# Performance work log

Hardware: AMD Instinct MI355X
Metric: run time of the kernel (lower is better)

Reference implementation:

```python
import jax, jax.numpy as jnp
import numpy as np

LN_EPS = 1e-5

def _layernorm(x, g, b):
    mu = jnp.mean(x, axis=-1, keepdims=True)
    var = jnp.var(x, axis=-1, keepdims=True)
    return (x - mu) / jnp.sqrt(var + LN_EPS) * g + b

def setup_inputs() -> dict:
    key = jax.random.key(0)
    ks = jax.random.split(key, 12)
    N, D_WSI, D_OMIC, D, DH = 50000, 1024, 1577, 256, 128
    def rn(k, shape, s=0.02):
        return jax.random.normal(k, shape, jnp.float32) * s
    return {
        'wsi': jax.random.normal(ks[0], (N, D_WSI), jnp.float32),
        'x_omic': jax.random.normal(ks[1], (D_OMIC,), jnp.float32),
        # SNNOmics: Linear(1577,256)+ELU, Linear(256,256)+ELU (AlphaDropout=eval identity)
        'W1': rn(ks[2], (D_OMIC, 256)), 'b1': jnp.zeros((256,), jnp.float32),
        'W2': rn(ks[3], (256, 256)), 'b2': jnp.zeros((256,), jnp.float32),
        # wsi projection Linear(1024,256)
        'Wp': rn(ks[4], (D_WSI, D)), 'bp': jnp.zeros((D,), jnp.float32),
        # MMAttentionLayer pre-norm (dim=256)
        'ln1_g': jnp.ones((D,), jnp.float32), 'ln1_b': jnp.zeros((D,), jnp.float32),
        # to_qkv: Linear(256, 3*heads*dim_head) = Linear(256, 384), no bias (heads=1, dim_head=128)
        'Wqkv': rn(ks[5], (D, 3 * DH)),
        # FeedForward(dim=128, mult=1): LN + Linear(128,128)+GELU+Linear(128,128) (no residual)
        'ln2_g': jnp.ones((DH,), jnp.float32), 'ln2_b': jnp.zeros((DH,), jnp.float32),
        'Wf1': rn(ks[6], (DH, DH)), 'bf1': jnp.zeros((DH,), jnp.float32),
        'Wf2': rn(ks[7], (DH, DH)), 'bf2': jnp.zeros((DH,), jnp.float32),
        # final LayerNorm(128)
        'ln3_g': jnp.ones((DH,), jnp.float32), 'ln3_b': jnp.zeros((DH,), jnp.float32),
        # to_logits: Linear(256,64)+ReLU+Linear(64,4)
        'Wl1': rn(ks[8], (2 * DH, 64)), 'bl1': jnp.zeros((64,), jnp.float32),
        'Wl2': rn(ks[9], (64, 4)), 'bl2': jnp.zeros((4,), jnp.float32),
    }

def reference(wsi, x_omic, W1, b1, W2, b2, Wp, bp, ln1_g, ln1_b, Wqkv,
              ln2_g, ln2_b, Wf1, bf1, Wf2, bf2, ln3_g, ln3_b, Wl1, bl1, Wl2, bl2):
    M = 1            # num_pathways
    DH = 128         # dim_head (heads=1)
    scale = DH ** -0.5
    # SNN omics encoder -> one pathway token [1, 256]
    h = jax.nn.elu(x_omic @ W1 + b1)
    h = jax.nn.elu(h @ W2 + b2)
    h_omic = h[None, :]                              # [1, 256]
    # WSI projection -> histology tokens [N, 256]
    wsi_embed = wsi @ Wp + bp                        # [N, 256]
    tokens = jnp.concatenate([h_omic, wsi_embed], axis=0)   # [1+N, 256]
    # MMAttentionLayer: pre-norm then asymmetric pathway/histology attention
    xn = _layernorm(tokens, ln1_g, ln1_b)
    qkv = xn @ Wqkv                                  # [1+N, 384]
    q, k, v = jnp.split(qkv, 3, axis=-1)             # each [1+N, 128]
    q = q * scale
    q_p, q_h = q[:M], q[M:]                          # [1,128], [N,128]
    k_p, k_h = k[:M], k[M:]
    # cross attention: histology -> pathways (rows of length M=1)
    cross_attn_hist = q_h @ k_p.T                    # [N, 1]
    cross_attn_hist = jax.nn.softmax(cross_attn_hist, axis=-1)
    # pathway row attends to [pathways | histology]
    attn_p = q_p @ k_p.T                             # [1, 1]
    cross_attn_p = q_p @ k_h.T                       # [1, N]
    attn_ph = jax.nn.softmax(jnp.concatenate([attn_p, cross_attn_p], axis=-1), axis=-1)  # [1, 1+N]
    out_p = attn_ph @ v                              # [1, 128]
    out_h = cross_attn_hist @ v[:M]                  # [N, 128]
    out = jnp.concatenate([out_p, out_h], axis=0)    # [1+N, 128] (residual=False: no conv)
    # FeedForward (no residual add in original) + LayerNorm
    mm = _layernorm(out, ln2_g, ln2_b)
    mm = jax.nn.gelu(mm @ Wf1 + bf1, approximate=False) @ Wf2 + bf2
    mm = _layernorm(mm, ln3_g, ln3_b)                # [1+N, 128]
    paths_embed = jnp.mean(mm[:M], axis=0)           # [128]
    wsi_embed_post = jnp.mean(mm[M:], axis=0)        # [128]
    embedding = jnp.concatenate([paths_embed, wsi_embed_post])[None, :]  # [1, 256]
    logits = jax.nn.relu(embedding @ Wl1 + bl1) @ Wl2 + bl2              # [1, 4]
    prob = jax.nn.softmax(logits, axis=-1)
    return logits, prob
```

## Files before the change

### kernel.cpp

```cpp
#include <hip/hip_runtime.h>
#include <hip/hip_bf16.h>
#include <math.h>

#define LN_EPS 1e-5f

typedef unsigned short ushortT;
typedef short bf16x8 __attribute__((ext_vector_type(8)));
typedef float f32x4 __attribute__((ext_vector_type(4)));

#define WS_QP   0
#define WS_V0   128
#define WS_S0   256
#define WS_LL   258
#define WS_E0   259
#define WS_H1P  512
#define WS_PART 4608
#define PART_STRIDE 132
#define PART_M 128
#define PART_L 129
#define WS_WTS  108000
#define WS_GP   109000
#define NCOMB   32
#define WS_WPT  131072
#define WS_WKVT 262144

__device__ __forceinline__ float elu1(float x){ return x > 0.f ? x : expm1f(x); }
__device__ __forceinline__ unsigned short f2bf(float x){
  unsigned u = __float_as_uint(x);
  return (unsigned short)((u + 0x7fffu + ((u >> 16) & 1u)) >> 16);
}
__device__ __forceinline__ unsigned pk2(float lo, float hi){
  union { __hip_bfloat162 h; unsigned u; } cv;
  cv.h = __float22bfloat162_rn(make_float2(lo, hi));
  return cv.u;
}
__device__ __forceinline__ void dma16(const void* g, void* l) {
  __builtin_amdgcn_global_load_lds(
      (const __attribute__((address_space(1))) unsigned int*)g,
      (__attribute__((address_space(3))) unsigned int*)l, 16, 0, 0);
}

__global__ __launch_bounds__(256) void k_prep(const float* __restrict__ Wp,
    const float* __restrict__ Wqkv, ushortT* __restrict__ wpt, ushortT* __restrict__ wkvt)
{
  int bb = blockIdx.x, t = threadIdx.x;
  if (bb < 256) {
    int k0 = bb * 4;
    unsigned lo, hi;
    lo = (unsigned)f2bf(Wp[(size_t)(k0 + 0) * 256 + t]) |
         ((unsigned)f2bf(Wp[(size_t)(k0 + 1) * 256 + t]) << 16);
    hi = (unsigned)f2bf(Wp[(size_t)(k0 + 2) * 256 + t]) |
         ((unsigned)f2bf(Wp[(size_t)(k0 + 3) * 256 + t]) << 16);
    *(uint2*)&wpt[t * 1024 + k0] = make_uint2(lo, hi);
  } else {
    int k0 = (bb - 256) * 4;
    unsigned lo, hi;
    lo = (unsigned)f2bf(Wqkv[(size_t)(k0 + 0) * 384 + 128 + t]) |
         ((unsigned)f2bf(Wqkv[(size_t)(k0 + 1) * 384 + 128 + t]) << 16);
    hi = (unsigned)f2bf(Wqkv[(size_t)(k0 + 2) * 384 + 128 + t]) |
         ((unsigned)f2bf(Wqkv[(size_t)(k0 + 3) * 384 + 128 + t]) << 16);
    *(uint2*)&wkvt[t * 256 + k0] = make_uint2(lo, hi);
  }
}

__global__ __launch_bounds__(256) void k_h1(const float* __restrict__ x,
    const float* __restrict__ W1, int d_omic, float* __restrict__ ws)
{
  int g = blockIdx.x, tid = threadIdx.x;
  int i0 = g * 99, i1 = min(i0 + 99, d_omic);
  __shared__ float xs[112];
  for (int i = i0 + tid; i < i1; i += 256) xs[i - i0] = x[i];
  __syncthreads();
  float s = 0.f;
  for (int i = i0; i < i1; i++) s = fmaf(xs[i - i0], W1[(size_t)i * 256 + tid], s);
  ws[WS_H1P + g * 256 + tid] = s;
}

__global__ __launch_bounds__(256) void k_omic(
    const float* __restrict__ b1,
    const float* __restrict__ W2, const float* __restrict__ b2,
    const float* __restrict__ Wqkv,
    const float* __restrict__ ln1_g, const float* __restrict__ ln1_b,
    float* __restrict__ ws)
{
  __shared__ float h1[256];
  __shared__ float xn0[256];
  __shared__ float qs[128], ks[128];
  __shared__ float red[8];
  int tid = threadIdx.x, lane = tid & 63, wave = tid >> 6;

  float s = b1[tid];
  for (int g = 0; g < 16; g++) s += ws[WS_H1P + g * 256 + tid];
  h1[tid] = elu1(s);
  __syncthreads();

  s = b2[tid];
  for (int i = 0; i < 256; i++) s = fmaf(h1[i], W2[i * 256 + tid], s);
  float t0 = elu1(s);

  float ps = t0, pq = t0 * t0;
  for (int m = 1; m < 64; m <<= 1) { ps += __shfl_xor(ps, m); pq += __shfl_xor(pq, m); }
  if (lane == 0) { red[wave] = ps; red[4 + wave] = pq; }
  __syncthreads();
  float mu = (red[0] + red[1] + red[2] + red[3]) * (1.f / 256.f);
  float var = (red[4] + red[5] + red[6] + red[7]) * (1.f / 256.f) - mu * mu;
  float xn = (t0 - mu) * rsqrtf(var + LN_EPS) * ln1_g[tid] + ln1_b[tid];
  xn0[tid] = xn;
  __syncthreads();

  float a = 0.f;
  for (int j = 0; j < 256; j++) a = fmaf(xn0[j], Wqkv[j * 384 + tid], a);
  if (tid < 128) { float q = a * 0.088388347648318447f; qs[tid] = q; ws[WS_QP + tid] = q; }
  else           { ks[tid - 128] = a; }
  if (tid < 128) {
    float av = 0.f;
    for (int j = 0; j < 256; j++) av = fmaf(xn0[j], Wqkv[j * 384 + 256 + tid], av);
    ws[WS_V0 + tid] = av;
  }
  __syncthreads();
  float p = (tid < 128) ? qs[tid] * ks[tid] : 0.f;
  for (int m = 1; m < 64; m <<= 1) p += __shfl_xor(p, m);
  if (lane == 0) red[wave] = p;
  __syncthreads();
  if (tid == 0) ws[WS_S0] = red[0] + red[1] + red[2] + red[3];
}

__global__ __launch_bounds__(256, 3) void k_main(
    const float* __restrict__ wsi, int N,
    const ushortT* __restrict__ wpt, const ushortT* __restrict__ wkvt,
    const float* __restrict__ bp,
    const float* __restrict__ ln1_g, const float* __restrict__ ln1_b,
    float* __restrict__ ws)
{
  __shared__ __align__(16) char R1[16384];
  __shared__ __align__(16) char R2[32768];
  __shared__ float wtsL[64];

  const int tid = threadIdx.x;
  const int lane = tid & 63, wv = tid >> 6;
  const int l15 = lane & 15, lh = lane >> 4;
  const int b = blockIdx.x, r0 = b * 64;

  int wgoff[4];
  #pragma unroll
  for (int i = 0; i < 4; ++i) {
    int row = 16 * wv + 4 * i + (lane >> 4);
    int c16 = lane & 15;
    int c16g = (((c16 >> 1) ^ (row & 7)) << 1) | (c16 & 1);
    int gr = r0 + row; gr = (gr < N) ? gr : (N - 1);
    wgoff[i] = gr * 1024 + c16g * 4;
  }
  const int pbase = (64 * wv + (lane >> 3)) * 1024 + (((lane & 7) ^ ((lane >> 3) & 7)) * 8);
  const int kbase = (64 * wv + (lane >> 2)) * 256 + (((lane & 3) ^ ((lane >> 2) & 3)) * 8);

  const f32x4 z4 = {0.f, 0.f, 0.f, 0.f};
  f32x4 acc[4][4];
  #pragma unroll
  for (int mt = 0; mt < 4; ++mt)
    #pragma unroll
    for (int nt = 0; nt < 4; ++nt) acc[mt][nt] = z4;

  bool rowbad[4];
  #pragma unroll
  for (int nt = 0; nt < 4; ++nt) rowbad[nt] = (r0 + l15 + 16 * nt) >= N;

  #pragma unroll
  for (int i = 0; i < 4; ++i) dma16(wsi + wgoff[i], R1 + (16 * wv + 4 * i) * 256);
  #pragma unroll
  for (int i = 0; i < 8; ++i) dma16(wpt + pbase + i * 8192, R2 + (64 * wv + 8 * i) * 128);
  __syncthreads();

  for (int s = 0; s < 16; ++s) {
    #pragma unroll
    for (int kc = 0; kc < 2; ++kc) {
      bf16x8 af[4], bfr[4];
      #pragma unroll
      for (int mt = 0; mt < 4; ++mt)
        af[mt] = *(const bf16x8*)(R2 + (64 * wv + 16 * mt + l15) * 128 +
                                  (((lh + 4 * kc) ^ (l15 & 7)) << 4));
      #pragma unroll
      for (int nt = 0; nt < 4; ++nt) {
        int row = l15 + 16 * nt;
        const char* p = R1 + row * 256 + (((lh + 4 * kc) ^ (row & 7)) << 5);
        uint4 ua = *(const uint4*)p;
        uint4 ub = *(const uint4*)(p + 16);
        if (rowbad[nt]) { ua = make_uint4(0,0,0,0); ub = make_uint4(0,0,0,0); }
        union { unsigned u[4]; bf16x8 v; } cv;
        cv.u[0] = pk2(__uint_as_float(ua.x), __uint_as_float(ua.y));
        cv.u[1] = pk2(__uint_as_float(ua.z), __uint_as_float(ua.w));
        cv.u[2] = pk2(__uint_as_float(ub.x), __uint_as_float(ub.y));
        cv.u[3] = pk2(__uint_as_float(ub.z), __uint_as_float(ub.w));
        bfr[nt] = cv.v;
      }
      #pragma unroll
      for (int mt = 0; mt < 4; ++mt)
        #pragma unroll
        for (int nt = 0; nt < 4; ++nt)
          acc[mt][nt] = __builtin_amdgcn_mfma_f32_16x16x32_bf16(af[mt], bfr[nt], acc[mt][nt], 0, 0, 0);
    }
    __syncthreads();
    if (s < 15) {
      #pragma unroll
      for (int i = 0; i < 4; ++i)
        dma16(wsi + wgoff[i] + (s + 1) * 64, R1 + (16 * wv + 4 * i) * 256);
      #pragma unroll
      for (int i = 0; i < 8; ++i)
        dma16(wpt + pbase + i * 8192 + (s + 1) * 64, R2 + (64 * wv + 8 * i) * 128);
    }
    __syncthreads();
  }

  float* red = (float*)R1;
  float4 bp4[4], g4[4], b4[4];
  #pragma unroll
  for (int mt = 0; mt < 4; ++mt) {
    int m0 = 64 * wv + 16 * mt + 4 * lh;
    bp4[mt] = *(const float4*)&bp[m0];
    g4[mt]  = *(const float4*)&ln1_g[m0];
    b4[mt]  = *(const float4*)&ln1_b[m0];
  }
  float ps[4], pq[4];
  #pragma unroll
  for (int nt = 0; nt < 4; ++nt) { ps[nt] = 0.f; pq[nt] = 0.f; }
  #pragma unroll
  for (int mt = 0; mt < 4; ++mt) {
    const float bb4[4] = {bp4[mt].x, bp4[mt].y, bp4[mt].z, bp4[mt].w};
    #pragma unroll
    for (int nt = 0; nt < 4; ++nt)
      #pragma unroll
      for (int r = 0; r < 4; ++r) {
        float v = acc[mt][nt][r] + bb4[r];
        acc[mt][nt][r] = v;
        ps[nt] += v; pq[nt] += v * v;
      }
  }
  #pragma unroll
  for (int nt = 0; nt < 4; ++nt) {
    ps[nt] += __shfl_xor(ps[nt], 16); pq[nt] += __shfl_xor(pq[nt], 16);
    ps[nt] += __shfl_xor(ps[nt], 32); pq[nt] += __shfl_xor(pq[nt], 32);
  }
  if (lh == 0) {
    #pragma unroll
    for (int nt = 0; nt < 4; ++nt) {
      int row = l15 + 16 * nt;
      red[(wv * 64 + row) * 2]     = ps[nt];
      red[(wv * 64 + row) * 2 + 1] = pq[nt];
    }
  }
  __syncthreads();
  float mu[4], rstd[4];
  #pragma unroll
  for (int nt = 0; nt < 4; ++nt) {
    int row = l15 + 16 * nt;
    float s_ = 0.f, q_ = 0.f;
    #pragma unroll
    for (int w2 = 0; w2 < 4; ++w2) { s_ += red[(w2 * 64 + row) * 2]; q_ += red[(w2 * 64 + row) * 2 + 1]; }
    float m_ = s_ * (1.f / 256.f);
    float v_ = q_ * (1.f / 256.f) - m_ * m_;
    mu[nt] = m_; rstd[nt] = rsqrtf(v_ + LN_EPS);
  }
  #pragma unroll
  for (int nt = 0; nt < 4; ++nt) {
    int row = l15 + 16 * nt;
    unsigned rswz = (unsigned)((row & 7) << 4);
    #pragma unroll
    for (int mt = 0; mt < 4; ++mt) {
      float x0 = (acc[mt][nt][0] - mu[nt]) * rstd[nt] * g4[mt].x + b4[mt].x;
      float x1 = (acc[mt][nt][1] - mu[nt]) * rstd[nt] * g4[mt].y + b4[mt].y;
      float x2 = (acc[mt][nt][2] - mu[nt]) * rstd[nt] * g4[mt].z + b4[mt].z;
      float x3 = (acc[mt][nt][3] - mu[nt]) * rstd[nt] * g4[mt].w + b4[mt].w;
      unsigned p0 = pk2(x0, x1);
      unsigned p1 = pk2(x2, x3);
      int m0 = 64 * wv + 16 * mt + 4 * lh;
      unsigned off = (unsigned)(row * 512 + m0 * 2) ^ rswz;
      *(uint2*)(R2 + off) = make_uint2(p0, p1);
    }
  }

  f32x4 acc2[4][4];
  #pragma unroll
  for (int mt = 0; mt < 4; ++mt)
    #pragma unroll
    for (int nt = 0; nt < 4; ++nt) acc2[mt][nt] = z4;

  for (int kk = 0; kk < 8; ++kk) {
    __syncthreads();
    #pragma unroll
    for (int i = 0; i < 4; ++i)
      dma16(wkvt + kbase + i * 4096 + kk * 32, R1 + (64 * wv + 16 * i) * 64);
    __syncthreads();
    bf16x8 af[4], bfr[4];
    #pragma unroll
    for (int mt = 0; mt < 4; ++mt)
      af[mt] = *(const bf16x8*)(R1 + (64 * wv + 16 * mt + l15) * 64 + ((lh ^ (l15 & 3)) << 4));
    #pragma unroll
    for (int nt = 0; nt < 4; ++nt) {
      int row = l15 + 16 * nt;
      unsigned off = (unsigned)(row * 512 + lh * 16 + kk * 64) ^ (unsigned)((row & 7) << 4);
      bfr[nt] = *(const bf16x8*)(R2 + off);
    }
    #pragma unroll
    for (int mt = 0; mt < 4; ++mt)
      #pragma unroll
      for (int nt = 0; nt < 4; ++nt)
        acc2[mt][nt] = __builtin_amdgcn_mfma_f32_16x16x32_bf16(af[mt], bfr[nt], acc2[mt][nt], 0, 0, 0);
  }
  __syncthreads();

  float* part = ws + WS_PART + (size_t)b * PART_STRIDE;

  if (wv < 2) {
    float4 qp4[4];
    #pragma unroll
    for (int mt = 0; mt < 4; ++mt)
      qp4[mt] = *(const float4*)&ws[WS_QP + 64 * wv + 16 * mt + 4 * lh];
    float sp[4];
    #pragma unroll
    for (int nt = 0; nt < 4; ++nt) {
      float s_ = 0.f;
      #pragma unroll
      for (int mt = 0; mt < 4; ++mt) {
        s_ = fmaf(qp4[mt].x, acc2[mt][nt][0], s_);
        s_ = fmaf(qp4[mt].y, acc2[mt][nt][1], s_);
        s_ = fmaf(qp4[mt].z, acc2[mt][nt][2], s_);
        s_ = fmaf(qp4[mt].w, acc2[mt][nt][3], s_);
      }
      sp[nt] = s_;
    }
    #pragma unroll
    for (int nt = 0; nt < 4; ++nt) {
      sp[nt] += __shfl_xor(sp[nt], 16);
      sp[nt] += __shfl_xor(sp[nt], 32);
    }
    if (lh == 0) {
      #pragma unroll
      for (int nt = 0; nt < 4; ++nt) red[wv * 64 + 16 * nt + l15] = sp[nt];
    }
  }
  __syncthreads();
  if (tid < 64) {
    int gr = r0 + tid;
    float s_ = red[tid] + red[64 + tid];
    if (gr >= N) s_ = -INFINITY;
    float mb = s_;
    #pragma unroll
    for (int m = 1; m < 64; m <<= 1) mb = fmaxf(mb, __shfl_xor(mb, m));
    float e = (gr < N) ? expf(s_ - mb) : 0.f;
    float l_ = e;
    #pragma unroll
    for (int m = 1; m < 64; m <<= 1) l_ += __shfl_xor(l_, m);
    wtsL[tid] = e;
    if (tid == 0) { part[PART_M] = mb; part[PART_L] = l_; }
  }
  __syncthreads();
  if (wv >= 2) {
    int wv2 = wv - 2;
    float wr[4];
    #pragma unroll
    for (int nt = 0; nt < 4; ++nt) wr[nt] = wtsL[16 * nt + l15];
    #pragma unroll
    for (int mt = 0; mt < 4; ++mt) {
      float vs0 = 0.f, vs1 = 0.f, vs2 = 0.f, vs3 = 0.f;
      #pragma unroll
      for (int nt = 0; nt < 4; ++nt) {
        vs0 = fmaf(wr[nt], acc2[mt][nt][0], vs0);
        vs1 = fmaf(wr[nt], acc2[mt][nt][1], vs1);
        vs2 = fmaf(wr[nt], acc2[mt][nt][2], vs2);
        vs3 = fmaf(wr[nt], acc2[mt][nt][3], vs3);
      }
      #pragma unroll
      for (int m = 1; m < 16; m <<= 1) {
        vs0 += __shfl_xor(vs0, m); vs1 += __shfl_xor(vs1, m);
        vs2 += __shfl_xor(vs2, m); vs3 += __shfl_xor(vs3, m);
      }
      if (l15 == 0)
        *(float4*)&part[64 * wv2 + 16 * mt + 4 * lh] = make_float4(vs0, vs1, vs2, vs3);
    }
  }
}

__global__ __launch_bounds__(256) void k_fin0(float* __restrict__ ws, int NB)
{
  __shared__ float red[8];
  int tid = threadIdx.x, lane = tid & 63, wave = tid >> 6;
  const float* part = ws + WS_PART;
  float s0 = ws[WS_S0];

  float mloc = s0;
  for (int bb = tid; bb < NB; bb += 256) mloc = fmaxf(mloc, part[(size_t)bb * PART_STRIDE + PART_M]);
  for (int m = 1; m < 64; m <<= 1) mloc = fmaxf(mloc, __shfl_xor(mloc, m));
  if (lane == 0) red[wave] = mloc;
  __syncthreads();
  float M = fmaxf(fmaxf(red[0], red[1]), fmaxf(red[2], red[3]));

  float lp = 0.f;
  for (int bb = tid; bb < NB; bb += 256) {
    float w = expf(part[(size_t)bb * PART_STRIDE + PART_M] - M);
    ws[WS_WTS + bb] = w;
    lp = fmaf(part[(size_t)bb * PART_STRIDE + PART_L], w, lp);
  }
  for (int m = 1; m < 64; m <<= 1) lp += __shfl_xor(lp, m);
  __syncthreads();
  if (lane == 0) red[wave] = lp;
  __syncthreads();
  if (tid == 0) {
    float e0 = expf(s0 - M);
    ws[WS_LL] = red[0] + red[1] + red[2] + red[3] + e0;
    ws[WS_E0] = e0;
  }
}

__global__ __launch_bounds__(128) void k_fin1(float* __restrict__ ws, int NB, int chunk)
{
  int g = blockIdx.x, col = threadIdx.x;
  int c0 = g * chunk, c1 = min(c0 + chunk, NB);
  const float* part = ws + WS_PART;
  const float* wts = ws + WS_WTS;
  float a = 0.f;
  #pragma unroll 4
  for (int bb = c0; bb < c1; ++bb)
    a = fmaf(part[(size_t)bb * PART_STRIDE + col], wts[bb], a);
  ws[WS_GP + g * 128 + col] = a;
}

__global__ __launch_bounds__(256) void k_final(
    const float* __restrict__ ws,
    const float* __restrict__ Wf1, const float* __restrict__ bf1,
    const float* __restrict__ Wf2, const float* __restrict__ bf2,
    const float* __restrict__ ln2_g, const float* __restrict__ ln2_b,
    const float* __restrict__ ln3_g, const float* __restrict__ ln3_b,
    const float* __restrict__ Wl1, const float* __restrict__ bl1,
    const float* __restrict__ Wl2, const float* __restrict__ bl2,
    float* __restrict__ out)
{
  __shared__ float rowb[2][128];
  __shared__ float mmb[2][128];
  __shared__ float red[8];
  __shared__ float emb[256];
  __shared__ float abuf[64];
  __shared__ float lbuf[4];
  int tid = threadIdx.x, lane = tid & 63, wave = tid >> 6;

  if (tid < 128) {
    float v0 = ws[WS_V0 + tid];
    float a = v0 * ws[WS_E0];
    #pragma unroll
    for (int g = 0; g < NCOMB; ++g) a += ws[WS_GP + g * 128 + tid];
    rowb[0][tid] = a / ws[WS_LL];
    rowb[1][tid] = v0;
  }
  __syncthreads();

  int row = tid >> 7, k = tid & 127;
  float x = rowb[row][k];
  float ps = x, pq = x * x;
  for (int m = 1; m < 64; m <<= 1) { ps += __shfl_xor(ps, m); pq += __shfl_xor(pq, m); }
  __syncthreads();
  if (lane == 0) { red[wave] = ps; red[4 + wave] = pq; }
  __syncthreads();
  {
    float sum = red[row * 2] + red[row * 2 + 1];
    float sq  = red[4 + row * 2] + red[4 + row * 2 + 1];
    float mu = sum * (1.f / 128.f);
    float var = sq * (1.f / 128.f) - mu * mu;
    x = (x - mu) * rsqrtf(var + LN_EPS) * ln2_g[k] + ln2_b[k];
  }
  mmb[row][k] = x;
  __syncthreads();
  float t1 = bf1[k];
  for (int j = 0; j < 128; j++) t1 = fmaf(mmb[row][j], Wf1[j * 128 + k], t1);
  float gg = t1 * 0.5f * (1.f + erff(t1 * 0.70710678118654752f));
  __syncthreads();
  rowb[row][k] = gg;
  __syncthreads();
  float t2 = bf2[k];
  for (int j = 0; j < 128; j++) t2 = fmaf(rowb[row][j], Wf2[j * 128 + k], t2);
  ps = t2; pq = t2 * t2;
  for (int m = 1; m < 64; m <<= 1) { ps += __shfl_xor(ps, m); pq += __shfl_xor(pq, m); }
  __syncthreads();
  if (lane == 0) { red[wave] = ps; red[4 + wave] = pq; }
  __syncthreads();
  {
    float sum = red[row * 2] + red[row * 2 + 1];
    float sq  = red[4 + row * 2] + red[4 + row * 2 + 1];
    float mu = sum * (1.f / 128.f);
    float var = sq * (1.f / 128.f) - mu * mu;
    t2 = (t2 - mu) * rsqrtf(var + LN_EPS) * ln3_g[k] + ln3_b[k];
  }
  emb[row * 128 + k] = t2;
  __syncthreads();
  if (tid < 64) {
    float a = bl1[tid];
    for (int j = 0; j < 256; j++) a = fmaf(emb[j], Wl1[j * 64 + tid], a);
    abuf[tid] = fmaxf(a, 0.f);
  }
  __syncthreads();
  if (tid < 4) {
    float lg = bl2[tid];
    for (int j = 0; j < 64; j++) lg = fmaf(abuf[j], Wl2[j * 4 + tid], lg);
    lbuf[tid] = lg;
  }
  __syncthreads();
  if (tid < 4) {
    float m4 = fmaxf(fmaxf(lbuf[0], lbuf[1]), fmaxf(lbuf[2], lbuf[3]));
    float e0 = expf(lbuf[0] - m4), e1 = expf(lbuf[1] - m4);
    float e2 = expf(lbuf[2] - m4), e3 = expf(lbuf[3] - m4);
    float ssum = e0 + e1 + e2 + e3;
    out[tid] = lbuf[tid];
    out[4 + tid] = expf(lbuf[tid] - m4) / ssum;
  }
}

extern "C" void kernel_launch(void* const* d_in, const int* in_sizes, int n_in,
                              void* d_out, int out_size, void* d_ws, size_t ws_size,
                              hipStream_t stream) {
  const float* wsi    = (const float*)d_in[0];
  const float* x_omic = (const float*)d_in[1];
  const float* W1     = (const float*)d_in[2];
  const float* b1     = (const float*)d_in[3];
  const float* W2     = (const float*)d_in[4];
  const float* b2     = (const float*)d_in[5];
  const float* Wp     = (const float*)d_in[6];
  const float* bp     = (const float*)d_in[7];
  const float* ln1_g  = (const float*)d_in[8];
  const float* ln1_b  = (const float*)d_in[9];
  const float* Wqkv   = (const float*)d_in[10];
  const float* ln2_g  = (const float*)d_in[11];
  const float* ln2_b  = (const float*)d_in[12];
  const float* Wf1    = (const float*)d_in[13];
  const float* bf1    = (const float*)d_in[14];
  const float* Wf2    = (const float*)d_in[15];
  const float* bf2    = (const float*)d_in[16];
  const float* ln3_g  = (const float*)d_in[17];
  const float* ln3_b  = (const float*)d_in[18];
  const float* Wl1    = (const float*)d_in[19];
  const float* bl1    = (const float*)d_in[20];
  const float* Wl2    = (const float*)d_in[21];
  const float* bl2    = (const float*)d_in[22];
  float* ws   = (float*)d_ws;
  float* outp = (float*)d_out;
  ushortT* wpt  = (ushortT*)(ws + WS_WPT);
  ushortT* wkvt = (ushortT*)(ws + WS_WKVT);

  int N = in_sizes[0] / 1024;
  int d_omic = in_sizes[1];
  int NB = (N + 63) / 64;
  int chunk = (NB + NCOMB - 1) / NCOMB;

  k_prep<<<320, 256, 0, stream>>>(Wp, Wqkv, wpt, wkvt);
  k_h1<<<16, 256, 0, stream>>>(x_omic, W1, d_omic, ws);
  k_omic<<<1, 256, 0, stream>>>(b1, W2, b2, Wqkv, ln1_g, ln1_b, ws);
  k_main<<<NB, 256, 0, stream>>>(wsi, N, wpt, wkvt, bp, ln1_g, ln1_b, ws);
  k_fin0<<<1, 256, 0, stream>>>(ws, NB);
  k_fin1<<<NCOMB, 128, 0, stream>>>(ws, NB, chunk);
  k_final<<<1, 256, 0, stream>>>(ws, Wf1, bf1, Wf2, bf2, ln2_g, ln2_b,
                                 ln3_g, ln3_b, Wl1, bl1, Wl2, bl2, outp);
}
```

Baseline: 160.3 us.

## Triple-buffer projection GEMM loads and double-buffer KV weight staging with explicit waitcnt

The main GEMM loop changes from a single-buffered 64-wide K step, with two full barriers per step, to a three-slot ring of 32-wide K chunks. Each ring slot is refilled by async global-to-LDS loads, and explicit vmcnt waits let loads for later chunks stay in flight during compute. The KV projection loop is likewise double-buffered, with its first loads issued before the layernorm epilogue. LDS use rises to about 72KB, so launch bounds drop from 3 to 2 blocks per CU, trading occupancy for overlap. The out-of-range row zero masking was removed, and rows past N now rely on the clamped duplicate-row loads.

Result: no change. 162.3 us (+1.3%).

```diff
diff --git a/kernel.cpp b/kernel.cpp
--- a/kernel.cpp
+++ b/kernel.cpp
@@ -39,6 +39,14 @@
       (const __attribute__((address_space(1))) unsigned int*)g,
       (__attribute__((address_space(3))) unsigned int*)l, 16, 0, 0);
 }
+template<int N> __device__ __forceinline__ void vwait() {
+  asm volatile("s_waitcnt vmcnt(%0)" :: "i"(N) : "memory");
+}
+__device__ __forceinline__ void lwait0() {
+  asm volatile("s_waitcnt lgkmcnt(0)" ::: "memory");
+}
+__device__ __forceinline__ void sbar()   { __builtin_amdgcn_s_barrier(); }
+__device__ __forceinline__ void schedb() { __builtin_amdgcn_sched_barrier(0); }
 
 __global__ __launch_bounds__(256) void k_prep(const float* __restrict__ Wp,
     const float* __restrict__ Wqkv, ushortT* __restrict__ wpt, ushortT* __restrict__ wkvt)
@@ -125,15 +133,15 @@
   if (tid == 0) ws[WS_S0] = red[0] + red[1] + red[2] + red[3];
 }
 
-__global__ __launch_bounds__(256, 3) void k_main(
+__global__ __launch_bounds__(256, 2) void k_main(
     const float* __restrict__ wsi, int N,
     const ushortT* __restrict__ wpt, const ushortT* __restrict__ wkvt,
     const float* __restrict__ bp,
     const float* __restrict__ ln1_g, const float* __restrict__ ln1_b,
     float* __restrict__ ws)
 {
-  __shared__ __align__(16) char R1[16384];
-  __shared__ __align__(16) char R2[32768];
+  __shared__ __align__(16) char SW[3 * 16384];
+  __shared__ __align__(16) char SS[3 * 8192];
   __shared__ float wtsL[64];
 
   const int tid = threadIdx.x;
@@ -141,17 +149,28 @@
   const int l15 = lane & 15, lh = lane >> 4;
   const int b = blockIdx.x, r0 = b * 64;
 
-  int wgoff[4];
-  #pragma unroll
-  for (int i = 0; i < 4; ++i) {
-    int row = 16 * wv + 4 * i + (lane >> 4);
-    int c16 = lane & 15;
-    int c16g = (((c16 >> 1) ^ (row & 7)) << 1) | (c16 & 1);
-    int gr = r0 + row; gr = (gr < N) ? gr : (N - 1);
-    wgoff[i] = gr * 1024 + c16g * 4;
-  }
-  const int pbase = (64 * wv + (lane >> 3)) * 1024 + (((lane & 7) ^ ((lane >> 3) & 7)) * 8);
-  const int kbase = (64 * wv + (lane >> 2)) * 256 + (((lane & 3) ^ ((lane >> 2) & 3)) * 8);
+  int wsrc[2];
+  #pragma unroll
+  for (int i = 0; i < 2; ++i) {
+    int row = 16 * wv + 8 * i + (lane >> 3);
+    int c   = lane & 7;
+    int gr  = r0 + row; gr = (gr < N) ? gr : (N - 1);
+    wsrc[i] = gr * 1024 + ((c ^ (row & 7)) << 2);
+  }
+  int psrc[4], kvsrc[4];
+  #pragma unroll
+  for (int j = 0; j < 4; ++j) {
+    int p  = lane >> 3;
+    int cc = (lane & 7) ^ (p & 7);
+    int mj = 16 * j + 2 * p + (cc >> 2);
+    int m  = 64 * wv + mj;
+    int c  = cc & 3;
+    psrc[j]  = m * 1024 + c * 8;
+    kvsrc[j] = m * 256  + c * 8;
+  }
+  const unsigned afc = (unsigned)(((4 * (l15 & 1) + lh) ^ (l15 >> 1)) << 4);
+  const unsigned bc0 = (unsigned)(((2 * lh)     ^ (l15 & 7)) << 4);
+  const unsigned bc1 = (unsigned)(((2 * lh + 1) ^ (l15 & 7)) << 4);
 
   const f32x4 z4 = {0.f, 0.f, 0.f, 0.f};
   f32x4 acc[4][4];
@@ -160,57 +179,59 @@
     #pragma unroll
     for (int nt = 0; nt < 4; ++nt) acc[mt][nt] = z4;
 
-  bool rowbad[4];
-  #pragma unroll
-  for (int nt = 0; nt < 4; ++nt) rowbad[nt] = (r0 + l15 + 16 * nt) >= N;
-
-  #pragma unroll
-  for (int i = 0; i < 4; ++i) dma16(wsi + wgoff[i], R1 + (16 * wv + 4 * i) * 256);
-  #pragma unroll
-  for (int i = 0; i < 8; ++i) dma16(wpt + pbase + i * 8192, R2 + (64 * wv + 8 * i) * 128);
-  __syncthreads();
-
-  for (int s = 0; s < 16; ++s) {
-    #pragma unroll
-    for (int kc = 0; kc < 2; ++kc) {
-      bf16x8 af[4], bfr[4];
-      #pragma unroll
-      for (int mt = 0; mt < 4; ++mt)
-        af[mt] = *(const bf16x8*)(R2 + (64 * wv + 16 * mt + l15) * 128 +
-                                  (((lh + 4 * kc) ^ (l15 & 7)) << 4));
-      #pragma unroll
-      for (int nt = 0; nt < 4; ++nt) {
-        int row = l15 + 16 * nt;
-        const char* p = R1 + row * 256 + (((lh + 4 * kc) ^ (row & 7)) << 5);
-        uint4 ua = *(const uint4*)p;
-        uint4 ub = *(const uint4*)(p + 16);
-        if (rowbad[nt]) { ua = make_uint4(0,0,0,0); ub = make_uint4(0,0,0,0); }
-        union { unsigned u[4]; bf16x8 v; } cv;
-        cv.u[0] = pk2(__uint_as_float(ua.x), __uint_as_float(ua.y));
-        cv.u[1] = pk2(__uint_as_float(ua.z), __uint_as_float(ua.w));
-        cv.u[2] = pk2(__uint_as_float(ub.x), __uint_as_float(ub.y));
-        cv.u[3] = pk2(__uint_as_float(ub.z), __uint_as_float(ub.w));
-        bfr[nt] = cv.v;
-      }
-      #pragma unroll
-      for (int mt = 0; mt < 4; ++mt)
-        #pragma unroll
-        for (int nt = 0; nt < 4; ++nt)
-          acc[mt][nt] = __builtin_amdgcn_mfma_f32_16x16x32_bf16(af[mt], bfr[nt], acc[mt][nt], 0, 0, 0);
-    }
-    __syncthreads();
-    if (s < 15) {
-      #pragma unroll
-      for (int i = 0; i < 4; ++i)
-        dma16(wsi + wgoff[i] + (s + 1) * 64, R1 + (16 * wv + 4 * i) * 256);
-      #pragma unroll
-      for (int i = 0; i < 8; ++i)
-        dma16(wpt + pbase + i * 8192 + (s + 1) * 64, R2 + (64 * wv + 8 * i) * 128);
-    }
-    __syncthreads();
-  }
-
-  float* red = (float*)R1;
+  auto stageP1 = [&](int kc, int slot) {
+    char* ds = SS + slot * 8192 + wv * 2048;
+    #pragma unroll
+    for (int i = 0; i < 2; ++i) dma16(wsi + wsrc[i] + kc * 32, ds + i * 1024);
+    char* dw = SW + slot * 16384 + wv * 4096;
+    #pragma unroll
+    for (int j = 0; j < 4; ++j) dma16(wpt + psrc[j] + kc * 32, dw + j * 1024);
+  };
+  auto computeP1 = [&](int slot) {
+    const char* Wb = SW + slot * 16384 + wv * 4096;
+    const char* Sb = SS + slot * 8192;
+    bf16x8 af[4], bfr[4];
+    #pragma unroll
+    for (int mt = 0; mt < 4; ++mt)
+      af[mt] = *(const bf16x8*)(Wb + (8 * mt + (l15 >> 1)) * 128 + afc);
+    #pragma unroll
+    for (int nt = 0; nt < 4; ++nt) {
+      const char* p = Sb + (l15 + 16 * nt) * 128;
+      uint4 ua = *(const uint4*)(p + bc0);
+      uint4 ub = *(const uint4*)(p + bc1);
+      union { unsigned u[4]; bf16x8 v; } cv;
+      cv.u[0] = pk2(__uint_as_float(ua.x), __uint_as_float(ua.y));
+      cv.u[1] = pk2(__uint_as_float(ua.z), __uint_as_float(ua.w));
+      cv.u[2] = pk2(__uint_as_float(ub.x), __uint_as_float(ub.y));
+      cv.u[3] = pk2(__uint_as_float(ub.z), __uint_as_float(ub.w));
+      bfr[nt] = cv.v;
+    }
+    #pragma unroll
+    for (int mt = 0; mt < 4; ++mt)
+      #pragma unroll
+      for (int nt = 0; nt < 4; ++nt)
+        acc[mt][nt] = __builtin_amdgcn_mfma_f32_16x16x32_bf16(af[mt], bfr[nt], acc[mt][nt], 0, 0, 0);
+  };
+
+  stageP1(0, 0); stageP1(1, 1); stageP1(2, 2);
+  int slot = 0;
+  for (int kc = 0; kc < 32; ++kc) {
+    if (kc < 30) vwait<12>(); else if (kc == 30) vwait<6>(); else vwait<0>();
+    sbar(); schedb();
+    computeP1(slot);
+    sbar(); schedb();
+    if (kc < 29) stageP1(kc + 3, slot);
+    slot = (slot == 2) ? 0 : slot + 1;
+  }
+
+  auto stageKV = [&](int t) {
+    char* dst = ((t & 1) ? SS : SW + 32768) + wv * 4096;
+    #pragma unroll
+    for (int j = 0; j < 4; ++j) dma16(wkvt + kvsrc[j] + t * 32, dst + j * 1024);
+  };
+  stageKV(0); stageKV(1);
+
+  float* red = (float*)(SS + 16384);
   float4 bp4[4], g4[4], b4[4];
   #pragma unroll
   for (int mt = 0; mt < 4; ++mt) {
@@ -247,7 +268,7 @@
       red[(wv * 64 + row) * 2 + 1] = pq[nt];
     }
   }
-  __syncthreads();
+  lwait0(); sbar(); schedb();
   float mu[4], rstd[4];
   #pragma unroll
   for (int nt = 0; nt < 4; ++nt) {
@@ -273,9 +294,10 @@
       unsigned p1 = pk2(x2, x3);
       int m0 = 64 * wv + 16 * mt + 4 * lh;
       unsigned off = (unsigned)(row * 512 + m0 * 2) ^ rswz;
-      *(uint2*)(R2 + off) = make_uint2(p0, p1);
-    }
-  }
+      *(uint2*)(SW + off) = make_uint2(p0, p1);
+    }
+  }
+  lwait0(); sbar(); schedb();
 
   f32x4 acc2[4][4];
   #pragma unroll
@@ -284,28 +306,29 @@
     for (int nt = 0; nt < 4; ++nt) acc2[mt][nt] = z4;
 
   for (int kk = 0; kk < 8; ++kk) {
-    __syncthreads();
-    #pragma unroll
-    for (int i = 0; i < 4; ++i)
-      dma16(wkvt + kbase + i * 4096 + kk * 32, R1 + (64 * wv + 16 * i) * 64);
-    __syncthreads();
-    bf16x8 af[4], bfr[4];
-    #pragma unroll
-    for (int mt = 0; mt < 4; ++mt)
-      af[mt] = *(const bf16x8*)(R1 + (64 * wv + 16 * mt + l15) * 64 + ((lh ^ (l15 & 3)) << 4));
-    #pragma unroll
-    for (int nt = 0; nt < 4; ++nt) {
-      int row = l15 + 16 * nt;
-      unsigned off = (unsigned)(row * 512 + lh * 16 + kk * 64) ^ (unsigned)((row & 7) << 4);
-      bfr[nt] = *(const bf16x8*)(R2 + off);
-    }
-    #pragma unroll
-    for (int mt = 0; mt < 4; ++mt)
-      #pragma unroll
-      for (int nt = 0; nt < 4; ++nt)
-        acc2[mt][nt] = __builtin_amdgcn_mfma_f32_16x16x32_bf16(af[mt], bfr[nt], acc2[mt][nt], 0, 0, 0);
-  }
-  __syncthreads();
+    if (kk < 7) vwait<4>(); else vwait<0>();
+    sbar(); schedb();
+    {
+      const char* Pb = ((kk & 1) ? SS : SW + 32768) + wv * 4096;
+      bf16x8 af[4], bfr[4];
+      #pragma unroll
+      for (int mt = 0; mt < 4; ++mt)
+        af[mt] = *(const bf16x8*)(Pb + (8 * mt + (l15 >> 1)) * 128 + afc);
+      #pragma unroll
+      for (int nt = 0; nt < 4; ++nt) {
+        int row = l15 + 16 * nt;
+        unsigned off = (unsigned)(row * 512 + lh * 16 + kk * 64) ^ (unsigned)((row & 7) << 4);
+        bfr[nt] = *(const bf16x8*)(SW + off);
+      }
+      #pragma unroll
+      for (int mt = 0; mt < 4; ++mt)
+        #pragma unroll
+        for (int nt = 0; nt < 4; ++nt)
+          acc2[mt][nt] = __builtin_amdgcn_mfma_f32_16x16x32_bf16(af[mt], bfr[nt], acc2[mt][nt], 0, 0, 0);
+    }
+    sbar(); schedb();
+    if (kk < 6) stageKV(kk + 2);
+  }
 
   float* part = ws + WS_PART + (size_t)b * PART_STRIDE;
 
```
